# Optimization experiments

Hardware: AMD Instinct MI355X
Metric: run time of the kernel (lower is better)

Reference implementation:

```python
import jax, jax.numpy as jnp
import numpy as np

N_NODES = 100000
N_EDGES = 1600000
D_IN = 128
D_OUT = 128


def setup_inputs() -> dict:
    key = jax.random.key(0)
    k1, k2, k3, k4 = jax.random.split(key, 4)
    x = jax.random.normal(k1, (N_NODES, D_IN), dtype=jnp.float32)
    edge_index = jax.random.randint(k2, (2, N_EDGES), 0, N_NODES, dtype=jnp.int64)
    # Xavier-uniform init as in the torch module
    limit = float(np.sqrt(6.0 / (D_IN + D_OUT)))
    self_weight = jax.random.uniform(k3, (D_IN, D_OUT), dtype=jnp.float32, minval=-limit, maxval=limit)
    neighbor_weight = jax.random.uniform(k4, (D_IN, D_OUT), dtype=jnp.float32, minval=-limit, maxval=limit)
    bias = jnp.zeros((D_OUT,), dtype=jnp.float32)
    return {"x": x, "edge_index": edge_index, "self_weight": self_weight,
            "neighbor_weight": neighbor_weight, "bias": bias}


def reference(x, edge_index, self_weight, neighbor_weight, bias):
    row, col = edge_index[0], edge_index[1]
    num_nodes = x.shape[0]
    # symmetric normalization: deg^-1/2 over rows, gathered per edge
    deg = jax.ops.segment_sum(jnp.ones_like(row, dtype=x.dtype), row,
                              num_segments=num_nodes)
    deg_inv_sqrt = deg ** -0.5
    norm = deg_inv_sqrt[row] * deg_inv_sqrt[col]  # [E]
    # dense transforms
    self_support = x @ self_weight                 # [N, D_OUT]
    h = x @ neighbor_weight                        # [N, D_OUT]
    # spmm: out[r] += norm_e * h[c] for each edge (r, c)
    msg = norm[:, None] * h[col]                   # [E, D_OUT]
    neighbor_support = jax.ops.segment_sum(msg, row, num_segments=num_nodes)
    return self_support + neighbor_support + bias
```

## Files before the change

### kernel.cpp

```cpp
#include <hip/hip_runtime.h>

#define N_NODES 100000
#define N_EDGES 1600000
#define D_FEAT 128
#define BUCKETS 256
#define RPB 391
#define BKCAP 8192
#define BIN_CHUNK 8192
#define BIN_WGS ((N_EDGES + BIN_CHUNK - 1) / BIN_CHUNK)

#define PRE_CONV_WGS (N_NODES * D_FEAT / 4 / 256)
#define PRE_WPREP_WGS 16
#define PRE_WGS (PRE_CONV_WGS + PRE_WPREP_WGS + BIN_WGS)

typedef unsigned int u32;
typedef unsigned short u16;
typedef __attribute__((ext_vector_type(8))) short bf16x8;
typedef __attribute__((ext_vector_type(4))) float f32x4;

__device__ inline float bfbits2f(u32 hi) { union { u32 u; float f; } v; v.u = hi; return v.f; }
__device__ inline float bflo(u32 pair) { return bfbits2f(pair << 16); }
__device__ inline float bfhi(u32 pair) { return bfbits2f(pair & 0xFFFF0000u); }
__device__ inline u16 f2bf(float f) {
  union { float f; u32 u; } v; v.f = f;
  u32 r = v.u + 0x7FFFu + ((v.u >> 16) & 1u);
  return (u16)(r >> 16);
}
__device__ inline int clampN(int v) { return ((unsigned)v < N_NODES) ? v : 0; }

__global__ __launch_bounds__(256) void k_pre(const float4* __restrict__ x4,
                                             uint2* __restrict__ xb2,
                                             const float* __restrict__ Wself,
                                             const float* __restrict__ Wnb,
                                             u16* __restrict__ Wbf,
                                             const int* __restrict__ ei,
                                             int* __restrict__ gcur,
                                             u32* __restrict__ binrec) {
  __shared__ int hist[BUCKETS], pref[BUCKETS], lcur[BUCKETS], gbase[BUCKETS];
  __shared__ u32 stag[BIN_CHUNK];
  __shared__ unsigned char sbkt[BIN_CHUNK];
  int b = blockIdx.x;
  int tid = threadIdx.x;
  if (b < PRE_CONV_WGS) {
    int i = b * 256 + tid;
    float4 v = x4[i];
    uint2 o;
    o.x = (u32)f2bf(v.x) | ((u32)f2bf(v.y) << 16);
    o.y = (u32)f2bf(v.z) | ((u32)f2bf(v.w) << 16);
    xb2[i] = o;
  } else if (b < PRE_CONV_WGS + PRE_WPREP_WGS) {
    int f = (b - PRE_CONV_WGS) * 256 + tid;
    int lane = f & 63, nt = (f >> 6) & 7, kk = (f >> 9) & 3, t = f >> 11;
    int q = lane >> 4, l16 = lane & 15;
    const float* W = t ? Wnb : Wself;
    int n = nt * 16 + l16;
    int k0 = (kk * 4 + q) * 8;
    u16 tmp[8];
#pragma unroll
    for (int j = 0; j < 8; j++) tmp[j] = f2bf(W[(k0 + j) * 128 + n]);
    uint4 o;
    o.x = (u32)tmp[0] | ((u32)tmp[1] << 16);
    o.y = (u32)tmp[2] | ((u32)tmp[3] << 16);
    o.z = (u32)tmp[4] | ((u32)tmp[5] << 16);
    o.w = (u32)tmp[6] | ((u32)tmp[7] << 16);
    *(uint4*)(Wbf + (long)f * 8) = o;
  } else {
    int wb = b - PRE_CONV_WGS - PRE_WPREP_WGS;
    long e0 = (long)wb * BIN_CHUNK;
    hist[tid] = 0;
    lcur[tid] = 0;
    __syncthreads();
    int rows[BIN_CHUNK / 256];
#pragma unroll
    for (int j = 0; j < BIN_CHUNK / 256; j++) {
      long e = e0 + j * 256 + tid;
      int r = (e < N_EDGES) ? clampN(ei[e]) : -1;
      rows[j] = r;
      if (r >= 0) atomicAdd(&hist[r / RPB], 1);
    }
    __syncthreads();
    int v = hist[tid];
    pref[tid] = v;
    __syncthreads();
    for (int off = 1; off < BUCKETS; off <<= 1) {
      int t = (tid >= off) ? pref[tid - off] : 0;
      __syncthreads();
      pref[tid] += t;
      __syncthreads();
    }
    int excl = pref[tid] - v;
    gbase[tid] = tid * BKCAP + atomicAdd(&gcur[tid], v);
    __syncthreads();
    pref[tid] = excl;
    __syncthreads();
#pragma unroll
    for (int j = 0; j < BIN_CHUNK / 256; j++) {
      int r = rows[j];
      if (r < 0) continue;
      long e = e0 + j * 256 + tid;
      int c = clampN(ei[N_EDGES + e]);
      int bk = r / RPB;
      int rl = r - bk * RPB;
      int pos = pref[bk] + atomicAdd(&lcur[bk], 1);
      stag[pos] = ((u32)rl << 17) | (u32)c;
      sbkt[pos] = (unsigned char)bk;
    }
    __syncthreads();
    int total = pref[BUCKETS - 1] + hist[BUCKETS - 1];
    for (int i = tid; i < total; i += 256) {
      int bk = sbkt[i];
      long idx = (long)gbase[bk] + (i - pref[bk]);
      if (idx < (long)(bk + 1) * BKCAP) binrec[idx] = stag[i];
    }
  }
}

__global__ __launch_bounds__(256) void k_csr(const int* __restrict__ gcur,
                                             const u32* __restrict__ binrec,
                                             int* __restrict__ deg,
                                             int* __restrict__ row_start,
                                             float* __restrict__ dis,
                                             int* __restrict__ cn) {
  __shared__ int h[512];
  __shared__ int ps[256];
  __shared__ int cur[512];
  __shared__ int win[BKCAP];
  int tid = threadIdx.x;
  int b = blockIdx.x;
  int r0 = b * RPB;
  int nrows = min(RPB, N_NODES - r0);
  long base = (long)b * BKCAP;
  int cnt = min(gcur[b], BKCAP);
  h[tid] = 0; h[tid + 256] = 0;
  __syncthreads();
  for (int i = tid; i < cnt; i += 256) {
    u32 rec = binrec[base + i];
    atomicAdd(&h[rec >> 17], 1);
  }
  __syncthreads();
  int s0 = h[2 * tid], s1 = h[2 * tid + 1];
  ps[tid] = s0 + s1;
  __syncthreads();
  int pv = ps[tid];
  for (int off = 1; off < 256; off <<= 1) {
    int t = (tid >= off) ? ps[tid - off] : 0;
    __syncthreads();
    ps[tid] += t;
    __syncthreads();
  }
  int pexcl = ps[tid] - pv;
  cur[2 * tid] = pexcl;
  cur[2 * tid + 1] = pexcl + s0;
  if (2 * tid < nrows) {
    int r = r0 + 2 * tid;
    deg[r] = s0;
    row_start[r] = (int)base + pexcl;
    dis[r] = s0 ? rsqrtf((float)s0) : 0.0f;
  }
  if (2 * tid + 1 < nrows) {
    int r = r0 + 2 * tid + 1;
    deg[r] = s1;
    row_start[r] = (int)base + pexcl + s0;
    dis[r] = s1 ? rsqrtf((float)s1) : 0.0f;
  }
  __syncthreads();
  for (int i = tid; i < cnt; i += 256) {
    u32 rec = binrec[base + i];
    int rl = rec >> 17;
    int p = atomicAdd(&cur[rl], 1);
    win[p] = (int)(rec & 0x1FFFF);
  }
  __syncthreads();
  for (int i = tid; i < cnt; i += 256) cn[base + i] = win[i];
}

__global__ __launch_bounds__(256) void k_agg(const int* __restrict__ row_start,
                                             const int* __restrict__ deg,
                                             const float* __restrict__ dis,
                                             const int* __restrict__ cn,
                                             const u32* __restrict__ xb ,
                                             u32* __restrict__ aggb) {
  int wave = threadIdx.x >> 6, lane = threadIdx.x & 63;
  int r = blockIdx.x * 4 + wave;
  if (r >= N_NODES) return;
  int start = row_start[r];
  int cnt = deg[r];
  float dr = dis[r];
  float a0 = 0.f, a1 = 0.f, b0 = 0.f, b1 = 0.f;
  int i = 0;
  for (; i + 8 <= cnt; i += 8) {
    int c[8];
    u32 g[8];
    float nc[8];
#pragma unroll
    for (int j = 0; j < 8; j++) c[j] = cn[start + i + j];
#pragma unroll
    for (int j = 0; j < 8; j++) g[j] = xb[(long)c[j] * 64 + lane];
#pragma unroll
    for (int j = 0; j < 8; j++) nc[j] = dis[c[j]];
#pragma unroll
    for (int j = 0; j < 8; j++) {
      float n = dr * nc[j];
      if (j & 1) { b0 += n * bflo(g[j]); b1 += n * bfhi(g[j]); }
      else       { a0 += n * bflo(g[j]); a1 += n * bfhi(g[j]); }
    }
  }
  for (; i + 2 <= cnt; i += 2) {
    int c0 = cn[start + i], c1 = cn[start + i + 1];
    u32 g0 = xb[(long)c0 * 64 + lane];
    u32 g1 = xb[(long)c1 * 64 + lane];
    float n0 = dr * dis[c0], n1 = dr * dis[c1];
    a0 += n0 * bflo(g0); a1 += n0 * bfhi(g0);
    b0 += n1 * bflo(g1); b1 += n1 * bfhi(g1);
  }
  if (i < cnt) {
    int c0 = cn[start + i];
    u32 g0 = xb[(long)c0 * 64 + lane];
    float n0 = dr * dis[c0];
    a0 += n0 * bflo(g0); a1 += n0 * bfhi(g0);
  }
  a0 += b0; a1 += b1;
  aggb[(long)r * 64 + lane] = (u32)f2bf(a0) | ((u32)f2bf(a1) << 16);
}

__global__ __launch_bounds__(256) void k_gemm(const u16* __restrict__ xb,
                                              const u16* __restrict__ aggb,
                                              const u16* __restrict__ Wbf,
                                              const float* __restrict__ bias,
                                              float* __restrict__ out) {
  int tid = threadIdx.x;
  int wave = tid >> 6, lane = tid & 63;
  int q = lane >> 4, l16 = lane & 15;
  int w0 = blockIdx.x * 128 + wave * 32;

  bf16x8 ax[2][4], ag[2][4];
#pragma unroll
  for (int mt = 0; mt < 2; mt++) {
    int node = w0 + mt * 16 + l16;
    long aoff = (long)clampN(node) * D_FEAT + q * 8;
#pragma unroll
    for (int kk = 0; kk < 4; kk++) {
      ax[mt][kk] = *(const bf16x8*)(xb + aoff + kk * 32);
      ag[mt][kk] = *(const bf16x8*)(aggb + aoff + kk * 32);
    }
  }

#pragma unroll
  for (int nt = 0; nt < 8; nt++) {
    bf16x8 bs[4], bn[4];
#pragma unroll
    for (int kk = 0; kk < 4; kk++) {
      bs[kk] = *(const bf16x8*)(Wbf + (long)(((0 * 4 + kk) * 8 + nt) * 64 + lane) * 8);
      bn[kk] = *(const bf16x8*)(Wbf + (long)(((1 * 4 + kk) * 8 + nt) * 64 + lane) * 8);
    }
    int ncol = nt * 16 + l16;
    float bv = bias[ncol];
#pragma unroll
    for (int mt = 0; mt < 2; mt++) {
      f32x4 acc = {0.f, 0.f, 0.f, 0.f};
#pragma unroll
      for (int kk = 0; kk < 4; kk++)
        acc = __builtin_amdgcn_mfma_f32_16x16x32_bf16(ax[mt][kk], bs[kk], acc, 0, 0, 0);
#pragma unroll
      for (int kk = 0; kk < 4; kk++)
        acc = __builtin_amdgcn_mfma_f32_16x16x32_bf16(ag[mt][kk], bn[kk], acc, 0, 0, 0);
#pragma unroll
      for (int reg = 0; reg < 4; reg++) {
        int node = w0 + mt * 16 + q * 4 + reg;
        if (node < N_NODES) out[(long)node * D_FEAT + ncol] = acc[reg] + bv;
      }
    }
  }
}

extern "C" void kernel_launch(void* const* d_in, const int* in_sizes, int n_in,
                              void* d_out, int out_size, void* d_ws, size_t ws_size,
                              hipStream_t stream) {
  const float* x = (const float*)d_in[0];
  const int* ei = (const int*)d_in[1];
  const float* Wself = (const float*)d_in[2];
  const float* Wnb = (const float*)d_in[3];
  const float* bias = (const float*)d_in[4];
  float* out = (float*)d_out;

  auto alignup = [](size_t v) { return (v + 511) & ~(size_t)511; };
  char* p = (char*)d_ws;
  int* deg = (int*)p;            p += alignup((size_t)N_NODES * 4);
  int* row_start = (int*)p;      p += alignup((size_t)N_NODES * 4);
  float* dis = (float*)p;        p += alignup((size_t)N_NODES * 4);
  int* gcur = (int*)p;           p += alignup((size_t)BUCKETS * 4);
  u16* Wbf = (u16*)p;            p += alignup((size_t)4096 * 8 * 2);
  int* cn = (int*)p;             p += alignup((size_t)BUCKETS * BKCAP * 4);
  u16* xb = (u16*)p;             p += alignup((size_t)N_NODES * D_FEAT * 2);
  u16* aggb = (u16*)p;           p += alignup((size_t)N_NODES * D_FEAT * 2);
  u32* binrec = (u32*)d_out;

  hipMemsetAsync(gcur, 0, (size_t)BUCKETS * 4, stream);

  k_pre<<<PRE_WGS, 256, 0, stream>>>((const float4*)x, (uint2*)xb, Wself, Wnb, Wbf, ei, gcur, binrec);
  k_csr<<<BUCKETS, 256, 0, stream>>>(gcur, binrec, deg, row_start, dis, cn);
  k_agg<<<(N_NODES + 3) / 4, 256, 0, stream>>>(row_start, deg, dis, cn, (const u32*)xb, (u32*)aggb);
  k_gemm<<<(N_NODES + 127) / 128, 256, 0, stream>>>(xb, aggb, Wbf, bias, out);
}
```

Baseline: 252.4 us.

## Use finer 1024-bucket binning with smaller chunks for CSR construction

Bucket count goes from 256 to 1024, so each bucket covers about 98 rows with a 2048-record capacity, and the binning chunk shrinks to 4096 edges. The CSR build now runs with four times as many smaller workgroups and a shorter 128-entry scan. The binning pass does a four-per-thread prefix scan and skips global atomics for empty buckets. The cost is more global atomics and scattered writes per chunk, and a higher chance that a bucket overflows its fixed capacity of 2048 records.

```diff
diff --git a/kernel.cpp b/kernel.cpp
--- a/kernel.cpp
+++ b/kernel.cpp
@@ -3,10 +3,10 @@
 #define N_NODES 100000
 #define N_EDGES 1600000
 #define D_FEAT 128
-#define BUCKETS 256
-#define RPB 391
-#define BKCAP 8192
-#define BIN_CHUNK 8192
+#define BUCKETS 1024
+#define RPB 98
+#define BKCAP 2048
+#define BIN_CHUNK 4096
 #define BIN_WGS ((N_EDGES + BIN_CHUNK - 1) / BIN_CHUNK)
 
 #define PRE_CONV_WGS (N_NODES * D_FEAT / 4 / 256)
@@ -36,9 +36,9 @@
                                              const int* __restrict__ ei,
                                              int* __restrict__ gcur,
                                              u32* __restrict__ binrec) {
-  __shared__ int hist[BUCKETS], pref[BUCKETS], lcur[BUCKETS], gbase[BUCKETS];
+  __shared__ int hist[BUCKETS], pref[BUCKETS], lcur[BUCKETS], ps[256];
   __shared__ u32 stag[BIN_CHUNK];
-  __shared__ unsigned char sbkt[BIN_CHUNK];
+  __shared__ u16 sbkt[BIN_CHUNK];
   int b = blockIdx.x;
   int tid = threadIdx.x;
   if (b < PRE_CONV_WGS) {
@@ -67,8 +67,7 @@
   } else {
     int wb = b - PRE_CONV_WGS - PRE_WPREP_WGS;
     long e0 = (long)wb * BIN_CHUNK;
-    hist[tid] = 0;
-    lcur[tid] = 0;
+    for (int k = tid; k < BUCKETS; k += 256) { hist[k] = 0; lcur[k] = 0; }
     __syncthreads();
     int rows[BIN_CHUNK / 256];
 #pragma unroll
@@ -79,19 +78,27 @@
       if (r >= 0) atomicAdd(&hist[r / RPB], 1);
     }
     __syncthreads();
-    int v = hist[tid];
-    pref[tid] = v;
-    __syncthreads();
-    for (int off = 1; off < BUCKETS; off <<= 1) {
-      int t = (tid >= off) ? pref[tid - off] : 0;
+    int v0 = hist[4 * tid + 0], v1 = hist[4 * tid + 1];
+    int v2 = hist[4 * tid + 2], v3 = hist[4 * tid + 3];
+    int s = v0 + v1 + v2 + v3;
+    ps[tid] = s;
+    __syncthreads();
+    for (int off = 1; off < 256; off <<= 1) {
+      int t = (tid >= off) ? ps[tid - off] : 0;
       __syncthreads();
-      pref[tid] += t;
+      ps[tid] += t;
       __syncthreads();
     }
-    int excl = pref[tid] - v;
-    gbase[tid] = tid * BKCAP + atomicAdd(&gcur[tid], v);
-    __syncthreads();
-    pref[tid] = excl;
+    int excl = ps[tid] - s;
+    pref[4 * tid + 0] = excl;
+    pref[4 * tid + 1] = excl + v0;
+    pref[4 * tid + 2] = excl + v0 + v1;
+    pref[4 * tid + 3] = excl + v0 + v1 + v2;
+    hist[4 * tid + 0] = (4 * tid + 0) * BKCAP + (v0 ? atomicAdd(&gcur[4 * tid + 0], v0) : 0);
+    hist[4 * tid + 1] = (4 * tid + 1) * BKCAP + (v1 ? atomicAdd(&gcur[4 * tid + 1], v1) : 0);
+    hist[4 * tid + 2] = (4 * tid + 2) * BKCAP + (v2 ? atomicAdd(&gcur[4 * tid + 2], v2) : 0);
+    hist[4 * tid + 3] = (4 * tid + 3) * BKCAP + (v3 ? atomicAdd(&gcur[4 * tid + 3], v3) : 0);
+    int total = ps[255];
     __syncthreads();
 #pragma unroll
     for (int j = 0; j < BIN_CHUNK / 256; j++) {
@@ -103,14 +110,13 @@
       int rl = r - bk * RPB;
       int pos = pref[bk] + atomicAdd(&lcur[bk], 1);
       stag[pos] = ((u32)rl << 17) | (u32)c;
-      sbkt[pos] = (unsigned char)bk;
-    }
-    __syncthreads();
-    int total = pref[BUCKETS - 1] + hist[BUCKETS - 1];
+      sbkt[pos] = (u16)bk;
+    }
+    __syncthreads();
     for (int i = tid; i < total; i += 256) {
       int bk = sbkt[i];
-      long idx = (long)gbase[bk] + (i - pref[bk]);
-      if (idx < (long)(bk + 1) * BKCAP) binrec[idx] = stag[i];
+      int idx = hist[bk] + (i - pref[bk]);
+      if (idx < (bk + 1) * BKCAP) binrec[idx] = stag[i];
     }
   }
 }
@@ -121,47 +127,37 @@
                                              int* __restrict__ row_start,
                                              float* __restrict__ dis,
                                              int* __restrict__ cn) {
-  __shared__ int h[512];
-  __shared__ int ps[256];
-  __shared__ int cur[512];
+  __shared__ int h[128];
+  __shared__ int cur[128];
   __shared__ int win[BKCAP];
   int tid = threadIdx.x;
   int b = blockIdx.x;
   int r0 = b * RPB;
-  int nrows = min(RPB, N_NODES - r0);
-  long base = (long)b * BKCAP;
-  int cnt = min(gcur[b], BKCAP);
-  h[tid] = 0; h[tid + 256] = 0;
+  int nrows = N_NODES - r0; if (nrows > RPB) nrows = RPB;
+  int base = b * BKCAP;
+  int cnt = gcur[b]; if (cnt > BKCAP) cnt = BKCAP;
+  if (tid < 128) h[tid] = 0;
   __syncthreads();
   for (int i = tid; i < cnt; i += 256) {
     u32 rec = binrec[base + i];
     atomicAdd(&h[rec >> 17], 1);
   }
   __syncthreads();
-  int s0 = h[2 * tid], s1 = h[2 * tid + 1];
-  ps[tid] = s0 + s1;
-  __syncthreads();
-  int pv = ps[tid];
-  for (int off = 1; off < 256; off <<= 1) {
-    int t = (tid >= off) ? ps[tid - off] : 0;
-    __syncthreads();
-    ps[tid] += t;
-    __syncthreads();
-  }
-  int pexcl = ps[tid] - pv;
-  cur[2 * tid] = pexcl;
-  cur[2 * tid + 1] = pexcl + s0;
-  if (2 * tid < nrows) {
-    int r = r0 + 2 * tid;
-    deg[r] = s0;
-    row_start[r] = (int)base + pexcl;
-    dis[r] = s0 ? rsqrtf((float)s0) : 0.0f;
-  }
-  if (2 * tid + 1 < nrows) {
-    int r = r0 + 2 * tid + 1;
-    deg[r] = s1;
-    row_start[r] = (int)base + pexcl + s0;
-    dis[r] = s1 ? rsqrtf((float)s1) : 0.0f;
+  int v = (tid < 128) ? h[tid] : 0;
+  __syncthreads();
+  for (int off = 1; off < 128; off <<= 1) {
+    int t = (tid >= off && tid < 128) ? h[tid - off] : 0;
+    __syncthreads();
+    if (tid < 128) h[tid] += t;
+    __syncthreads();
+  }
+  int excl = (tid < 128) ? (h[tid] - v) : 0;
+  if (tid < 128) cur[tid] = excl;
+  if (tid < nrows) {
+    int r = r0 + tid;
+    deg[r] = v;
+    row_start[r] = base + excl;
+    dis[r] = v ? rsqrtf((float)v) : 0.0f;
   }
   __syncthreads();
   for (int i = tid; i < cnt; i += 256) {
```

After: 258.0 us. 1.02x slower.
